# Kernel tuning notes

Hardware: AMD Instinct MI355X
Metric: run time of the kernel (lower is better)

The kernel has to match this reference:

```python
import jax, jax.numpy as jnp
import numpy as np

B, T, C, H = 2, 2048, 1024, 16
D = C // H  # head dim, even
NEG = -1e10  # masked_fill value used by the torch module (not -inf)


def _rope_cache(dim, max_positions):
    # Faithful to source: theta_i = 1/10000**(-2*(i-1)/dim), i = arange(dim//2)
    i = jnp.arange(dim // 2, dtype=jnp.float32)
    theta = 1.0 / (10000.0 ** (-2.0 * (i - 1.0) / dim))
    ang = jnp.arange(max_positions, dtype=jnp.float32)[:, None] * theta[None, :]  # [T, D/2]
    return jnp.cos(ang), jnp.sin(ang)


def _apply_rope(x, cos, sin):
    # x: [B,H,T,D]; consecutive pairs form complex numbers (x[...,2j], x[...,2j+1])
    xp = x.reshape(*x.shape[:-1], D // 2, 2)
    xr, xi = xp[..., 0], xp[..., 1]
    rr = xr * cos - xi * sin
    ri = xr * sin + xi * cos
    return jnp.stack([rr, ri], axis=-1).reshape(x.shape)


def setup_inputs() -> dict:
    key = jax.random.key(0)
    ks = jax.random.split(key, 5)
    s = 1.0 / np.sqrt(C)
    return {
        'x': jax.random.normal(ks[0], (B, T, C), jnp.float32),
        'Wq': jax.random.normal(ks[1], (C, C), jnp.float32) * s,
        'bq': jnp.zeros((C,), jnp.float32),
        'Wk': jax.random.normal(ks[2], (C, C), jnp.float32) * s,
        'bk': jnp.zeros((C,), jnp.float32),
        'Wv': jax.random.normal(ks[3], (C, C), jnp.float32) * s,
        'bv': jnp.zeros((C,), jnp.float32),
        'Wp': jax.random.normal(ks[4], (C, C), jnp.float32) * s,
        'bp': jnp.zeros((C,), jnp.float32),
    }


def reference(x, Wq, bq, Wk, bk, Wv, bv, Wp, bp):
    cos, sin = _rope_cache(D, T)  # [T, D/2]
    def split_heads(h):
        return h.reshape(B, T, H, D).transpose(0, 2, 1, 3)  # [B,H,T,D]
    q = split_heads(x @ Wq.T + bq)
    k = split_heads(x @ Wk.T + bk)
    v = split_heads(x @ Wv.T + bv)
    q = _apply_rope(q, cos, sin)
    k = _apply_rope(k, cos, sin)
    att = jnp.einsum('bhqd,bhkd->bhqk', q, k) * (1.0 / np.sqrt(D))  # [B,H,T,T]
    causal = jnp.tril(jnp.ones((T, T), bool))
    att = jnp.where(causal, att, NEG)
    att = jax.nn.softmax(att, axis=-1)
    y = jnp.einsum('bhqk,bhkd->bhqd', att, v)
    y = y.transpose(0, 2, 1, 3).reshape(B, T, C)
    return y @ Wp.T + bp
```

## Files before the change

kernel.cpp:

```cpp
#include <hip/hip_runtime.h>

#define SEQ 2048
#define CDIM 1024
#define NHEAD 16
#define HDIM 64
#define NSLOT 80

typedef __bf16 bf16x8 __attribute__((ext_vector_type(8)));
typedef __bf16 bf16x4v __attribute__((ext_vector_type(4)));
typedef float f32x4 __attribute__((ext_vector_type(4)));

typedef const __attribute__((address_space(1))) char* gcp_t;
typedef __attribute__((address_space(3))) char* lcp_t;

__device__ __forceinline__ void gload16(const void* g, void* l) {
    __builtin_amdgcn_global_load_lds((gcp_t)g, (lcp_t)l, 16, 0, 0);
}

__device__ __forceinline__ unsigned short f2bf(float f) {
    unsigned int u = __float_as_uint(f);
    u += 0x7fffu + ((u >> 16) & 1u);
    return (unsigned short)(u >> 16);
}

__device__ __forceinline__ float bflo(unsigned int u) { return __uint_as_float(u << 16); }
__device__ __forceinline__ float bfhi(unsigned int u) { return __uint_as_float(u & 0xffff0000u); }

__device__ __forceinline__ int swz16(int r) { return ((r >> 1) & 3) << 4; }


__global__ void cvt_kernel(const float* __restrict__ src, unsigned short* __restrict__ dst, int n4) {
    int i = blockIdx.x * blockDim.x + threadIdx.x;
    if (i < n4) {
        float4 v = ((const float4*)src)[i];
        ushort4 o;
        o.x = f2bf(v.x); o.y = f2bf(v.y); o.z = f2bf(v.z); o.w = f2bf(v.w);
        ((ushort4*)dst)[i] = o;
    }
}

__global__ void cvtw_kernel(const float* __restrict__ Wq, const float* __restrict__ Wk,
                            const float* __restrict__ Wv, const float* __restrict__ Wp,
                            unsigned short* __restrict__ wqkv, unsigned short* __restrict__ wpb) {
    int i = blockIdx.x * blockDim.x + threadIdx.x;
    int which = i >> 18, r = i & 262143;
    const float* s = (which == 0) ? Wq : (which == 1) ? Wk : (which == 2) ? Wv : Wp;
    unsigned short* d = (which < 3) ? (wqkv + (size_t)which * 1048576) : wpb;
    float4 v = ((const float4*)s)[r];
    ushort4 o;
    o.x = f2bf(v.x); o.y = f2bf(v.y); o.z = f2bf(v.z); o.w = f2bf(v.w);
    ((ushort4*)d)[r] = o;
}

__global__ void rope_kernel(float2* __restrict__ cstab) {
    int idx = blockIdx.x * blockDim.x + threadIdx.x;
    int j = idx & 31, t = idx >> 5;
    float e = -2.0f * ((float)j - 1.0f) / 64.0f;
    float denom = (float)pow(10000.0, (double)e);
    float theta = 1.0f / denom;
    float ang = (float)t * theta;
    cstab[idx] = make_float2(cosf(ang), sinf(ang));
}

template <int MODE, int BM, int NXT, int NYT>
__global__ __launch_bounds__(256) void gemm_bt(
    const unsigned short* __restrict__ A, const unsigned short* __restrict__ Bm,
    const float* __restrict__ b0, const float* __restrict__ b1, const float* __restrict__ b2,
    unsigned short* __restrict__ qb, unsigned short* __restrict__ kb,
    unsigned short* __restrict__ vtb, float* __restrict__ outf,
    const float2* __restrict__ cstab)
{
    constexpr int K = 1024;
    constexpr int NIT = K / 32;
    constexpr int NR = (BM == 128) ? 4 : 2;
    constexpr int ABYTES = BM * 64;
    constexpr int BBYTES = 128 * 64;
    __shared__ __align__(16) char As[3][ABYTES];
    __shared__ __align__(16) char Bs[3][BBYTES];
    const int tid = threadIdx.x, lane = tid & 63, wid = tid >> 6;
    constexpr int NWG = NXT * NYT;
    const int bid = blockIdx.x;
    const int swz = (bid & 7) * (NWG >> 3) + (bid >> 3);
    const int mt = swz / NXT;
    const int m0 = mt * BM, n0 = (swz - mt * NXT) * 128;
    const int wr = (BM == 128) ? ((wid >> 1) * 64) : 0;
    const int wc = (BM == 128) ? ((wid & 1) * 64) : (wid * 32);

    f32x4 acc[4][NR] = {};

    const char* Ag = (const char*)(A + (size_t)m0 * K);
    const char* Bg = (const char*)(Bm + (size_t)n0 * K);
    const int r0 = tid >> 2, cb = (tid & 3) * 16;
    const int ldsw = wid << 10;

    auto stage = [&](int k0, int bufi) {
        char* Ad = As[bufi];
        char* Bd = Bs[bufi];
        gload16(Ag + (size_t)r0 * 2048 + k0 * 2 + (cb ^ swz16(r0)), Ad + ldsw);
        if (BM == 128)
            gload16(Ag + (size_t)(r0 + 64) * 2048 + k0 * 2 + (cb ^ swz16(r0 + 64)), Ad + 4096 + ldsw);
        gload16(Bg + (size_t)r0 * 2048 + k0 * 2 + (cb ^ swz16(r0)), Bd + ldsw);
        gload16(Bg + (size_t)(r0 + 64) * 2048 + k0 * 2 + (cb ^ swz16(r0 + 64)), Bd + 4096 + ldsw);
    };

    stage(0, 0);
    stage(32, 1);

    int cur = 0;
    for (int it = 0; it < NIT; ++it) {
        if (it + 1 < NIT) {
            if constexpr (BM == 128) asm volatile("s_waitcnt vmcnt(4)" ::: "memory");
            else                     asm volatile("s_waitcnt vmcnt(3)" ::: "memory");
        } else {
            asm volatile("s_waitcnt vmcnt(0)" ::: "memory");
        }
        __builtin_amdgcn_s_barrier();
        asm volatile("" ::: "memory");
        if (it + 2 < NIT) {
            int nxt2 = cur + 2; if (nxt2 >= 3) nxt2 -= 3;
            stage((it + 2) * 32, nxt2);
        }
        const char* Ac = As[cur];
        const char* Bc = Bs[cur];
        const int fs = (lane >> 4) * 16;
        bf16x8 af[4], bfr[NR];
#pragma unroll
        for (int am = 0; am < 4; ++am) {
            const int r = wr + am * 16 + (lane & 15);
            af[am] = *(const bf16x8*)(Ac + r * 64 + (fs ^ swz16(r)));
        }
#pragma unroll
        for (int an = 0; an < NR; ++an) {
            const int r = wc + an * 16 + (lane & 15);
            bfr[an] = *(const bf16x8*)(Bc + r * 64 + (fs ^ swz16(r)));
        }
#pragma unroll
        for (int am = 0; am < 4; ++am)
#pragma unroll
            for (int an = 0; an < NR; ++an)
                acc[am][an] = __builtin_amdgcn_mfma_f32_16x16x32_bf16(af[am], bfr[an], acc[am][an], 0, 0, 0);
        cur = (cur == 2) ? 0 : cur + 1;
    }

    if (MODE == 0) {
        const float QSCL = 0.18033688011112042f;
#pragma unroll
        for (int an = 0; an < NR; ++an) {
            const int ng = n0 + wc + an * 16 + (lane & 15);
            const int which = ng >> 10, nl = ng & 1023;
            const int h = nl >> 6, d = nl & 63;
            const float* bptr = (which == 0) ? b0 : (which == 1) ? b1 : b2;
            const float bias = bptr[nl];
            if (which < 2) {
                unsigned short* dst = (which == 0) ? qb : kb;
                const float qs = (which == 0) ? QSCL : 1.0f;
                const int j = d >> 1;
#pragma unroll
                for (int am = 0; am < 4; ++am) {
#pragma unroll
                    for (int i = 0; i < 4; ++i) {
                        const int row = m0 + wr + am * 16 + (lane >> 4) * 4 + i;
                        const int bb = row >> 11, t = row & 2047;
                        float v = acc[am][an][i] + bias;
                        float p = __shfl_xor(v, 1);
                        const float2 cs = cstab[t * 32 + j];
                        v = (d & 1) ? fmaf(v, cs.x, p * cs.y) : fmaf(v, cs.x, -p * cs.y);
                        dst[((size_t)((bb * 16 + h) * 2048 + t)) * 64 + d] = f2bf(v * qs);
                    }
                }
            } else {
#pragma unroll
                for (int am = 0; am < 4; ++am) {
                    const int rowb = m0 + wr + am * 16 + (lane >> 4) * 4;
                    const int bb = rowb >> 11, t = rowb & 2047;
                    ushort4 pk;
                    pk.x = f2bf(acc[am][an][0] + bias);
                    pk.y = f2bf(acc[am][an][1] + bias);
                    pk.z = f2bf(acc[am][an][2] + bias);
                    pk.w = f2bf(acc[am][an][3] + bias);
                    *(ushort4*)(vtb + ((size_t)((bb * 16 + h) * 64 + d)) * 2048 + t) = pk;
                }
            }
        }
    } else {
#pragma unroll
        for (int an = 0; an < NR; ++an) {
            const int col = n0 + wc + an * 16 + (lane & 15);
            const float bias = b0[col];
#pragma unroll
            for (int am = 0; am < 4; ++am)
#pragma unroll
                for (int i = 0; i < 4; ++i) {
                    const int row = m0 + wr + am * 16 + (lane >> 4) * 4 + i;
                    outf[(size_t)row * 1024 + col] = acc[am][an][i] + bias;
                }
        }
    }
}

__global__ __launch_bounds__(256) void attn_kernel(
    const unsigned short* __restrict__ qb, const unsigned short* __restrict__ kb,
    const unsigned short* __restrict__ vtb, unsigned short* __restrict__ pb,
    float2* __restrict__ ml)
{
    __shared__ __align__(16) unsigned short Ks[2][64 * 64];
    __shared__ __align__(16) unsigned short Vs[2][64 * 64];
    __shared__ __align__(16) unsigned short Ps[4][16 * 64];
    const int tid = threadIdx.x, lane = tid & 63, wid = tid >> 6;
    const int bh = blockIdx.x;
    const int y = blockIdx.y;
    int qt, ck, nc;
    if (y < 32)      { qt = 31 - (y >> 2); ck = y & 3; nc = 4; }
    else if (y < 56) { int t2 = y - 32; int k3 = t2 / 3; qt = 23 - k3; ck = t2 - k3 * 3; nc = 3; }
    else if (y < 72) { int t2 = y - 56; qt = 15 - (t2 >> 1); ck = t2 & 1; nc = 2; }
    else             { qt = 7 - (y - 72); ck = 0; nc = 1; }
    const int nt = qt + 1;
    const int t0 = ck * nt / nc, t1 = (ck + 1) * nt / nc;
    const int q0 = qt * 64;
    const int qw = q0 + wid * 16;
    const unsigned short* Qg = qb + (size_t)bh * SEQ * HDIM;
    const char* Kg = (const char*)(kb + (size_t)bh * SEQ * HDIM);
    const char* Vg = (const char*)(vtb + (size_t)bh * HDIM * SEQ);

    bf16x8 qf[2];
#pragma unroll
    for (int kf = 0; kf < 2; ++kf)
        qf[kf] = *(const bf16x8*)(Qg + (size_t)(qw + (lane & 15)) * 64 + kf * 32 + (lane >> 4) * 8);

    f32x4 o[4] = {};
    float mrun = -3e38f;
    float lrun = 0.0f;

    const int cr0 = tid >> 3, cc0 = ((tid & 7) * 16) ^ ((cr0 & 7) << 4);
    const int cr1 = cr0 + 32, cc1 = ((tid & 7) * 16) ^ ((cr1 & 7) << 4);
    const int ldsw = wid << 10;

    auto stage = [&](int kt, int bufi) {
        const size_t kv0 = (size_t)kt * 64;
        gload16(Kg + (kv0 + cr0) * 128 + cc0, (char*)Ks[bufi] + ldsw);
        gload16(Kg + (kv0 + cr1) * 128 + cc1, (char*)Ks[bufi] + 4096 + ldsw);
        gload16(Vg + (size_t)cr0 * 4096 + kv0 * 2 + cc0, (char*)Vs[bufi] + ldsw);
        gload16(Vg + (size_t)cr1 * 4096 + kv0 * 2 + cc1, (char*)Vs[bufi] + 4096 + ldsw);
    };

    stage(t0, 0);
    __syncthreads();

    for (int kt = t0; kt < t1; ++kt) {
        const int cur = (kt - t0) & 1;
        if (kt + 1 < t1) stage(kt + 1, cur ^ 1);
        const int kv0 = kt * 64;
        {
            f32x4 s[4] = {};
            __builtin_amdgcn_s_setprio(1);
#pragma unroll
            for (int kf = 0; kf < 2; ++kf) {
                bf16x8 kfr[4];
#pragma unroll
                for (int an = 0; an < 4; ++an) {
                    const int r = an * 16 + (lane & 15);
                    kfr[an] = *(const bf16x8*)((const char*)Ks[cur] + r * 128 + ((kf * 64 + (lane >> 4) * 16) ^ ((r & 7) << 4)));
                }
#pragma unroll
                for (int an = 0; an < 4; ++an)
                    s[an] = __builtin_amdgcn_mfma_f32_16x16x32_bf16(kfr[an], qf[kf], s[an], 0, 0, 0);
            }
            __builtin_amdgcn_s_setprio(0);
            const bool need_mask = (kv0 + 63 > qw);
            const int qg = qw + (lane & 15);
            const int kbase = kv0 + ((lane >> 4) << 2);
            float p[4][4];
            float mx = -3e38f;
#pragma unroll
            for (int an = 0; an < 4; ++an)
#pragma unroll
                for (int i = 0; i < 4; ++i) {
                    float v = s[an][i];
                    if (need_mask && (kbase + an * 16 + i > qg)) v = -3e38f;
                    p[an][i] = v;
                    mx = fmaxf(mx, v);
                }
            mx = fmaxf(mx, __shfl_xor(mx, 16));
            mx = fmaxf(mx, __shfl_xor(mx, 32));
            if (!__all(mx <= mrun + 8.0f)) {
                const float mnew = fmaxf(mrun, mx);
                const float fsc = __builtin_amdgcn_exp2f(mrun - mnew);
                lrun *= fsc;
#pragma unroll
                for (int dn = 0; dn < 4; ++dn) o[dn] *= fsc;
                mrun = mnew;
            }
            float rs = 0.0f;
#pragma unroll
            for (int an = 0; an < 4; ++an)
#pragma unroll
                for (int i = 0; i < 4; ++i) {
                    p[an][i] = __builtin_amdgcn_exp2f(p[an][i] - mrun);
                    rs += p[an][i];
                }
            rs += __shfl_xor(rs, 16);
            rs += __shfl_xor(rs, 32);
            lrun += rs;
            const int ql = lane & 15;
            char* pbs = (char*)Ps[wid] + ql * 128;
            const int xr = (ql & 7) << 4;
            const int gb = (lane >> 4) << 3;
#pragma unroll
            for (int an = 0; an < 4; ++an) {
                bf16x4v pk;
                pk[0] = (__bf16)p[an][0]; pk[1] = (__bf16)p[an][1];
                pk[2] = (__bf16)p[an][2]; pk[3] = (__bf16)p[an][3];
                *(bf16x4v*)(pbs + ((an * 32 + gb) ^ xr)) = pk;
            }
            __builtin_amdgcn_s_setprio(1);
#pragma unroll
            for (int kf = 0; kf < 2; ++kf) {
                bf16x8 vf[4], pf;
#pragma unroll
                for (int dn = 0; dn < 4; ++dn) {
                    const int r = dn * 16 + (lane & 15);
                    vf[dn] = *(const bf16x8*)((const char*)Vs[cur] + r * 128 + ((kf * 64 + (lane >> 4) * 16) ^ ((r & 7) << 4)));
                }
                {
                    const int qlr = lane & 15;
                    pf = *(const bf16x8*)((const char*)Ps[wid] + qlr * 128 + ((kf * 64 + (lane >> 4) * 16) ^ ((qlr & 7) << 4)));
                }
#pragma unroll
                for (int dn = 0; dn < 4; ++dn)
                    o[dn] = __builtin_amdgcn_mfma_f32_16x16x32_bf16(vf[dn], pf, o[dn], 0, 0, 0);
            }
            __builtin_amdgcn_s_setprio(0);
        }
        __syncthreads();
    }

    {
        const size_t sbase = (size_t)bh * NSLOT + y;
        const int qloc = wid * 16 + (lane & 15);
        unsigned short* prow = pb + (sbase * 64 + qloc) * 64;
#pragma unroll
        for (int dn = 0; dn < 4; ++dn) {
            const int d = dn * 16 + ((lane >> 4) << 2);
            bf16x4v pk;
            pk[0] = (__bf16)o[dn][0];
            pk[1] = (__bf16)o[dn][1];
            pk[2] = (__bf16)o[dn][2];
            pk[3] = (__bf16)o[dn][3];
            *(bf16x4v*)(prow + d) = pk;
        }
        if ((lane >> 4) == 0) ml[sbase * 64 + qloc] = make_float2(mrun, lrun);
    }
}

__global__ __launch_bounds__(256) void combine_kernel(
    const unsigned short* __restrict__ pb, const float2* __restrict__ ml,
    unsigned short* __restrict__ yb)
{
    const int qt = blockIdx.x, bh = blockIdx.y;
    const int b = bh >> 4, h = bh & 15;
    int base, nc;
    if (qt >= 24)      { base = (31 - qt) * 4;      nc = 4; }
    else if (qt >= 16) { base = 32 + (23 - qt) * 3; nc = 3; }
    else if (qt >= 8)  { base = 56 + (15 - qt) * 2; nc = 2; }
    else               { base = 72 + (7 - qt);      nc = 1; }
    const int t = threadIdx.x;
    const int q = t >> 2;
    const int d0 = (t & 3) * 16;
    const size_t sbase = (size_t)bh * NSLOT + base;

    float m[4], l[4];
    float M = -3e38f;
#pragma unroll
    for (int c = 0; c < 4; ++c)
        if (c < nc) {
            float2 v = ml[(sbase + c) * 64 + q];
            m[c] = v.x; l[c] = v.y;
            M = fmaxf(M, v.x);
        }
    float L = 0.0f;
    float w[4];
#pragma unroll
    for (int c = 0; c < 4; ++c)
        if (c < nc) {
            w[c] = __builtin_amdgcn_exp2f(m[c] - M);
            L += l[c] * w[c];
        }
    const float invL = 1.0f / L;

    float acc[16] = {};
#pragma unroll
    for (int c = 0; c < 4; ++c)
        if (c < nc) {
            const float wc = w[c] * invL;
            const uint4* src = (const uint4*)(pb + ((sbase + c) * 64 + q) * 64 + d0);
            uint4 A = src[0], B = src[1];
            const unsigned int ua[8] = {A.x, A.y, A.z, A.w, B.x, B.y, B.z, B.w};
#pragma unroll
            for (int k = 0; k < 8; ++k) {
                acc[2 * k]     = fmaf(wc, bflo(ua[k]), acc[2 * k]);
                acc[2 * k + 1] = fmaf(wc, bfhi(ua[k]), acc[2 * k + 1]);
            }
        }

    unsigned int outw[8];
#pragma unroll
    for (int k = 0; k < 8; ++k)
        outw[k] = (unsigned int)f2bf(acc[2 * k]) | ((unsigned int)f2bf(acc[2 * k + 1]) << 16);
    uint4* dst = (uint4*)(yb + (size_t)(b * SEQ + qt * 64 + q) * CDIM + h * 64 + d0);
    dst[0] = make_uint4(outw[0], outw[1], outw[2], outw[3]);
    dst[1] = make_uint4(outw[4], outw[5], outw[6], outw[7]);
}


extern "C" void kernel_launch(void* const* d_in, const int* in_sizes, int n_in,
                              void* d_out, int out_size, void* d_ws, size_t ws_size,
                              hipStream_t stream) {
    (void)in_sizes; (void)n_in; (void)out_size; (void)ws_size;
    const float* x  = (const float*)d_in[0];
    const float* Wq = (const float*)d_in[1];
    const float* bq = (const float*)d_in[2];
    const float* Wk = (const float*)d_in[3];
    const float* bk = (const float*)d_in[4];
    const float* Wv = (const float*)d_in[5];
    const float* bv = (const float*)d_in[6];
    const float* Wp = (const float*)d_in[7];
    const float* bp = (const float*)d_in[8];
    float* out = (float*)d_out;

    char* ws = (char*)d_ws;
    size_t off = 0;
    auto take = [&](size_t bytes) -> char* {
        char* p = ws + off;
        off = (off + bytes + 255) & ~(size_t)255;
        return p;
    };
    float2* cstab = (float2*)take((size_t)SEQ * 32 * 8);
    unsigned short* xb   = (unsigned short*)take((size_t)4096 * 1024 * 2);
    unsigned short* wqkv = (unsigned short*)take((size_t)3 * 1024 * 1024 * 2);
    unsigned short* wpb  = (unsigned short*)take((size_t)1024 * 1024 * 2);
    unsigned short* qbuf = (unsigned short*)take((size_t)32 * SEQ * HDIM * 2);
    unsigned short* kbuf = (unsigned short*)take((size_t)32 * SEQ * HDIM * 2);
    unsigned short* vtb  = (unsigned short*)take((size_t)32 * HDIM * SEQ * 2);
    unsigned short* yb   = (unsigned short*)take((size_t)4096 * 1024 * 2);
    unsigned short* pbuf = (unsigned short*)take((size_t)32 * NSLOT * 64 * 64 * 2);
    float2* mlb          = (float2*)take((size_t)32 * NSLOT * 64 * 8);

    rope_kernel<<<256, 256, 0, stream>>>(cstab);
    cvt_kernel<<<4096, 256, 0, stream>>>(x, xb, 1048576);
    cvtw_kernel<<<4096, 256, 0, stream>>>(Wq, Wk, Wv, Wp, wqkv, wpb);

    gemm_bt<0, 128, 24, 32><<<768, 256, 0, stream>>>(xb, wqkv, bq, bk, bv, qbuf, kbuf, vtb, nullptr, cstab);
    dim3 g1(32, NSLOT);
    attn_kernel<<<g1, 256, 0, stream>>>(qbuf, kbuf, vtb, pbuf, mlb);
    dim3 gc(32, 32);
    combine_kernel<<<gc, 256, 0, stream>>>(pbuf, mlb, yb);
    gemm_bt<1, 64, 8, 64><<<512, 256, 0, stream>>>(yb, wpb, bp, nullptr, nullptr, nullptr, nullptr, nullptr, out, cstab);
}
```

Measured before the change: 146.8 us.

## Use 128-row query tiles in attention and simplify GEMM pipeline to double buffering

The attention kernel now gives each wave 32 query rows instead of 16, so every K/V tile loaded into shared memory serves twice as many queries and the split-KV slot count halves. Key tiles lying entirely above a wave's diagonal are skipped. The GEMM drops its 3-stage pipeline with manual vmcnt waits and its block-index swizzle, going back to a 2-stage double buffer with __syncthreads and a plain 2D grid. The GEMM change gives up load/compute overlap and L2 locality, and the larger attention tiles raise register pressure and lower the block count.

```diff
diff --git a/kernel.cpp b/kernel.cpp
--- a/kernel.cpp
+++ b/kernel.cpp
@@ -4,7 +4,7 @@
 #define CDIM 1024
 #define NHEAD 16
 #define HDIM 64
-#define NSLOT 80
+#define NSLOT 40
 
 typedef __bf16 bf16x8 __attribute__((ext_vector_type(8)));
 typedef __bf16 bf16x4v __attribute__((ext_vector_type(4)));
@@ -62,7 +62,7 @@
     cstab[idx] = make_float2(cosf(ang), sinf(ang));
 }
 
-template <int MODE, int BM, int NXT, int NYT>
+template <int MODE, int BM>
 __global__ __launch_bounds__(256) void gemm_bt(
     const unsigned short* __restrict__ A, const unsigned short* __restrict__ Bm,
     const float* __restrict__ b0, const float* __restrict__ b1, const float* __restrict__ b2,
@@ -73,16 +73,10 @@
     constexpr int K = 1024;
     constexpr int NIT = K / 32;
     constexpr int NR = (BM == 128) ? 4 : 2;
-    constexpr int ABYTES = BM * 64;
-    constexpr int BBYTES = 128 * 64;
-    __shared__ __align__(16) char As[3][ABYTES];
-    __shared__ __align__(16) char Bs[3][BBYTES];
+    __shared__ __align__(16) char As[2][BM * 64];
+    __shared__ __align__(16) char Bs[2][128 * 64];
     const int tid = threadIdx.x, lane = tid & 63, wid = tid >> 6;
-    constexpr int NWG = NXT * NYT;
-    const int bid = blockIdx.x;
-    const int swz = (bid & 7) * (NWG >> 3) + (bid >> 3);
-    const int mt = swz / NXT;
-    const int m0 = mt * BM, n0 = (swz - mt * NXT) * 128;
+    const int m0 = blockIdx.y * BM, n0 = blockIdx.x * 128;
     const int wr = (BM == 128) ? ((wid >> 1) * 64) : 0;
     const int wc = (BM == 128) ? ((wid & 1) * 64) : (wid * 32);
 
@@ -97,29 +91,18 @@
         char* Ad = As[bufi];
         char* Bd = Bs[bufi];
         gload16(Ag + (size_t)r0 * 2048 + k0 * 2 + (cb ^ swz16(r0)), Ad + ldsw);
-        if (BM == 128)
+        if constexpr (BM == 128)
             gload16(Ag + (size_t)(r0 + 64) * 2048 + k0 * 2 + (cb ^ swz16(r0 + 64)), Ad + 4096 + ldsw);
         gload16(Bg + (size_t)r0 * 2048 + k0 * 2 + (cb ^ swz16(r0)), Bd + ldsw);
         gload16(Bg + (size_t)(r0 + 64) * 2048 + k0 * 2 + (cb ^ swz16(r0 + 64)), Bd + 4096 + ldsw);
     };
 
     stage(0, 0);
-    stage(32, 1);
-
-    int cur = 0;
+    __syncthreads();
+
     for (int it = 0; it < NIT; ++it) {
-        if (it + 1 < NIT) {
-            if constexpr (BM == 128) asm volatile("s_waitcnt vmcnt(4)" ::: "memory");
-            else                     asm volatile("s_waitcnt vmcnt(3)" ::: "memory");
-        } else {
-            asm volatile("s_waitcnt vmcnt(0)" ::: "memory");
-        }
-        __builtin_amdgcn_s_barrier();
-        asm volatile("" ::: "memory");
-        if (it + 2 < NIT) {
-            int nxt2 = cur + 2; if (nxt2 >= 3) nxt2 -= 3;
-            stage((it + 2) * 32, nxt2);
-        }
+        const int cur = it & 1;
+        if (it + 1 < NIT) stage((it + 1) * 32, cur ^ 1);
         const char* Ac = As[cur];
         const char* Bc = Bs[cur];
         const int fs = (lane >> 4) * 16;
@@ -139,7 +122,7 @@
 #pragma unroll
             for (int an = 0; an < NR; ++an)
                 acc[am][an] = __builtin_amdgcn_mfma_f32_16x16x32_bf16(af[am], bfr[an], acc[am][an], 0, 0, 0);
-        cur = (cur == 2) ? 0 : cur + 1;
+        __syncthreads();
     }
 
     if (MODE == 0) {
@@ -205,31 +188,33 @@
 {
     __shared__ __align__(16) unsigned short Ks[2][64 * 64];
     __shared__ __align__(16) unsigned short Vs[2][64 * 64];
-    __shared__ __align__(16) unsigned short Ps[4][16 * 64];
+    __shared__ __align__(16) unsigned short Ps[4][32 * 64];
     const int tid = threadIdx.x, lane = tid & 63, wid = tid >> 6;
     const int bh = blockIdx.x;
     const int y = blockIdx.y;
     int qt, ck, nc;
-    if (y < 32)      { qt = 31 - (y >> 2); ck = y & 3; nc = 4; }
-    else if (y < 56) { int t2 = y - 32; int k3 = t2 / 3; qt = 23 - k3; ck = t2 - k3 * 3; nc = 3; }
-    else if (y < 72) { int t2 = y - 56; qt = 15 - (t2 >> 1); ck = t2 & 1; nc = 2; }
-    else             { qt = 7 - (y - 72); ck = 0; nc = 1; }
-    const int nt = qt + 1;
+    if (y < 16)      { qt = 15 - (y >> 2); ck = y & 3; nc = 4; }
+    else if (y < 28) { int t2 = y - 16; int k3 = t2 / 3; qt = 11 - k3; ck = t2 - k3 * 3; nc = 3; }
+    else if (y < 36) { int t2 = y - 28; qt = 7 - (t2 >> 1); ck = t2 & 1; nc = 2; }
+    else             { qt = 3 - (y - 36); ck = 0; nc = 1; }
+    const int nt = 2 * qt + 2;
     const int t0 = ck * nt / nc, t1 = (ck + 1) * nt / nc;
-    const int q0 = qt * 64;
-    const int qw = q0 + wid * 16;
+    const int q0 = qt * 128;
+    const int qw = q0 + wid * 32;
     const unsigned short* Qg = qb + (size_t)bh * SEQ * HDIM;
     const char* Kg = (const char*)(kb + (size_t)bh * SEQ * HDIM);
     const char* Vg = (const char*)(vtb + (size_t)bh * HDIM * SEQ);
 
-    bf16x8 qf[2];
-#pragma unroll
-    for (int kf = 0; kf < 2; ++kf)
-        qf[kf] = *(const bf16x8*)(Qg + (size_t)(qw + (lane & 15)) * 64 + kf * 32 + (lane >> 4) * 8);
-
-    f32x4 o[4] = {};
-    float mrun = -3e38f;
-    float lrun = 0.0f;
+    bf16x8 qf[2][2];
+#pragma unroll
+    for (int am = 0; am < 2; ++am)
+#pragma unroll
+        for (int kf = 0; kf < 2; ++kf)
+            qf[am][kf] = *(const bf16x8*)(Qg + (size_t)(qw + am * 16 + (lane & 15)) * 64 + kf * 32 + (lane >> 4) * 8);
+
+    f32x4 o[4][2] = {};
+    float mrun[2] = {-3e38f, -3e38f};
+    float lrun[2] = {0.0f, 0.0f};
 
     const int cr0 = tid >> 3, cc0 = ((tid & 7) * 16) ^ ((cr0 & 7) << 4);
     const int cr1 = cr0 + 32, cc1 = ((tid & 7) * 16) ^ ((cr1 & 7) << 4);
@@ -250,8 +235,8 @@
         const int cur = (kt - t0) & 1;
         if (kt + 1 < t1) stage(kt + 1, cur ^ 1);
         const int kv0 = kt * 64;
-        {
-            f32x4 s[4] = {};
+        if (kv0 <= qw + 31) {
+            f32x4 s[4][2] = {};
             __builtin_amdgcn_s_setprio(1);
 #pragma unroll
             for (int kf = 0; kf < 2; ++kf) {
@@ -263,71 +248,79 @@
                 }
 #pragma unroll
                 for (int an = 0; an < 4; ++an)
-                    s[an] = __builtin_amdgcn_mfma_f32_16x16x32_bf16(kfr[an], qf[kf], s[an], 0, 0, 0);
+#pragma unroll
+                    for (int am = 0; am < 2; ++am)
+                        s[an][am] = __builtin_amdgcn_mfma_f32_16x16x32_bf16(kfr[an], qf[am][kf], s[an][am], 0, 0, 0);
             }
             __builtin_amdgcn_s_setprio(0);
             const bool need_mask = (kv0 + 63 > qw);
-            const int qg = qw + (lane & 15);
-            const int kbase = kv0 + ((lane >> 4) << 2);
-            float p[4][4];
-            float mx = -3e38f;
-#pragma unroll
-            for (int an = 0; an < 4; ++an)
-#pragma unroll
-                for (int i = 0; i < 4; ++i) {
-                    float v = s[an][i];
-                    if (need_mask && (kbase + an * 16 + i > qg)) v = -3e38f;
-                    p[an][i] = v;
-                    mx = fmaxf(mx, v);
-                }
-            mx = fmaxf(mx, __shfl_xor(mx, 16));
-            mx = fmaxf(mx, __shfl_xor(mx, 32));
-            if (!__all(mx <= mrun + 8.0f)) {
-                const float mnew = fmaxf(mrun, mx);
-                const float fsc = __builtin_amdgcn_exp2f(mrun - mnew);
-                lrun *= fsc;
-#pragma unroll
-                for (int dn = 0; dn < 4; ++dn) o[dn] *= fsc;
-                mrun = mnew;
-            }
-            float rs = 0.0f;
-#pragma unroll
-            for (int an = 0; an < 4; ++an)
-#pragma unroll
-                for (int i = 0; i < 4; ++i) {
-                    p[an][i] = __builtin_amdgcn_exp2f(p[an][i] - mrun);
-                    rs += p[an][i];
-                }
-            rs += __shfl_xor(rs, 16);
-            rs += __shfl_xor(rs, 32);
-            lrun += rs;
-            const int ql = lane & 15;
-            char* pbs = (char*)Ps[wid] + ql * 128;
-            const int xr = (ql & 7) << 4;
-            const int gb = (lane >> 4) << 3;
-#pragma unroll
-            for (int an = 0; an < 4; ++an) {
-                bf16x4v pk;
-                pk[0] = (__bf16)p[an][0]; pk[1] = (__bf16)p[an][1];
-                pk[2] = (__bf16)p[an][2]; pk[3] = (__bf16)p[an][3];
-                *(bf16x4v*)(pbs + ((an * 32 + gb) ^ xr)) = pk;
+#pragma unroll
+            for (int am = 0; am < 2; ++am) {
+                const int qg = qw + am * 16 + (lane & 15);
+                const int kbase = kv0 + ((lane >> 4) << 2);
+                float p[4][4];
+                float mx = -3e38f;
+#pragma unroll
+                for (int an = 0; an < 4; ++an)
+#pragma unroll
+                    for (int i = 0; i < 4; ++i) {
+                        float v = s[an][am][i];
+                        if (need_mask && (kbase + an * 16 + i > qg)) v = -3e38f;
+                        p[an][i] = v;
+                        mx = fmaxf(mx, v);
+                    }
+                mx = fmaxf(mx, __shfl_xor(mx, 16));
+                mx = fmaxf(mx, __shfl_xor(mx, 32));
+                if (!__all(mx <= mrun[am] + 8.0f)) {
+                    const float mnew = fmaxf(mrun[am], mx);
+                    const float fsc = __builtin_amdgcn_exp2f(mrun[am] - mnew);
+                    lrun[am] *= fsc;
+#pragma unroll
+                    for (int dn = 0; dn < 4; ++dn) o[dn][am] *= fsc;
+                    mrun[am] = mnew;
+                }
+                float rs = 0.0f;
+#pragma unroll
+                for (int an = 0; an < 4; ++an)
+#pragma unroll
+                    for (int i = 0; i < 4; ++i) {
+                        p[an][i] = __builtin_amdgcn_exp2f(p[an][i] - mrun[am]);
+                        rs += p[an][i];
+                    }
+                rs += __shfl_xor(rs, 16);
+                rs += __shfl_xor(rs, 32);
+                lrun[am] += rs;
+                const int ql = am * 16 + (lane & 15);
+                char* pbs = (char*)Ps[wid] + ql * 128;
+                const int xr = (ql & 7) << 4;
+                const int gb = (lane >> 4) << 3;
+#pragma unroll
+                for (int an = 0; an < 4; ++an) {
+                    bf16x4v pk;
+                    pk[0] = (__bf16)p[an][0]; pk[1] = (__bf16)p[an][1];
+                    pk[2] = (__bf16)p[an][2]; pk[3] = (__bf16)p[an][3];
+                    *(bf16x4v*)(pbs + ((an * 32 + gb) ^ xr)) = pk;
+                }
             }
             __builtin_amdgcn_s_setprio(1);
 #pragma unroll
             for (int kf = 0; kf < 2; ++kf) {
-                bf16x8 vf[4], pf;
+                bf16x8 vf[4], pf[2];
 #pragma unroll
                 for (int dn = 0; dn < 4; ++dn) {
                     const int r = dn * 16 + (lane & 15);
                     vf[dn] = *(const bf16x8*)((const char*)Vs[cur] + r * 128 + ((kf * 64 + (lane >> 4) * 16) ^ ((r & 7) << 4)));
                 }
-                {
-                    const int qlr = lane & 15;
-                    pf = *(const bf16x8*)((const char*)Ps[wid] + qlr * 128 + ((kf * 64 + (lane >> 4) * 16) ^ ((qlr & 7) << 4)));
+#pragma unroll
+                for (int am = 0; am < 2; ++am) {
+                    const int ql = am * 16 + (lane & 15);
+                    pf[am] = *(const bf16x8*)((const char*)Ps[wid] + ql * 128 + ((kf * 64 + (lane >> 4) * 16) ^ ((ql & 7) << 4)));
                 }
 #pragma unroll
                 for (int dn = 0; dn < 4; ++dn)
-                    o[dn] = __builtin_amdgcn_mfma_f32_16x16x32_bf16(vf[dn], pf, o[dn], 0, 0, 0);
+#pragma unroll
+                    for (int am = 0; am < 2; ++am)
+                        o[dn][am] = __builtin_amdgcn_mfma_f32_16x16x32_bf16(vf[dn], pf[am], o[dn][am], 0, 0, 0);
             }
             __builtin_amdgcn_s_setprio(0);
         }
@@ -336,19 +329,22 @@
 
     {
         const size_t sbase = (size_t)bh * NSLOT + y;
-        const int qloc = wid * 16 + (lane & 15);
-        unsigned short* prow = pb + (sbase * 64 + qloc) * 64;
-#pragma unroll
-        for (int dn = 0; dn < 4; ++dn) {
-            const int d = dn * 16 + ((lane >> 4) << 2);
-            bf16x4v pk;
-            pk[0] = (__bf16)o[dn][0];
-            pk[1] = (__bf16)o[dn][1];
-            pk[2] = (__bf16)o[dn][2];
-            pk[3] = (__bf16)o[dn][3];
-            *(bf16x4v*)(prow + d) = pk;
-        }
-        if ((lane >> 4) == 0) ml[sbase * 64 + qloc] = make_float2(mrun, lrun);
+#pragma unroll
+        for (int am = 0; am < 2; ++am) {
+            const int qloc = wid * 32 + am * 16 + (lane & 15);
+            unsigned short* prow = pb + (sbase * 128 + qloc) * 64;
+#pragma unroll
+            for (int dn = 0; dn < 4; ++dn) {
+                const int d = dn * 16 + ((lane >> 4) << 2);
+                bf16x4v pk;
+                pk[0] = (__bf16)o[dn][am][0];
+                pk[1] = (__bf16)o[dn][am][1];
+                pk[2] = (__bf16)o[dn][am][2];
+                pk[3] = (__bf16)o[dn][am][3];
+                *(bf16x4v*)(prow + d) = pk;
+            }
+            if ((lane >> 4) == 0) ml[sbase * 128 + qloc] = make_float2(mrun[am], lrun[am]);
+        }
     }
 }
 
@@ -356,15 +352,16 @@
     const unsigned short* __restrict__ pb, const float2* __restrict__ ml,
     unsigned short* __restrict__ yb)
 {
-    const int qt = blockIdx.x, bh = blockIdx.y;
+    const int bx = blockIdx.x, bh = blockIdx.y;
+    const int qt = bx >> 1, qh = (bx & 1) * 64;
     const int b = bh >> 4, h = bh & 15;
     int base, nc;
-    if (qt >= 24)      { base = (31 - qt) * 4;      nc = 4; }
-    else if (qt >= 16) { base = 32 + (23 - qt) * 3; nc = 3; }
-    else if (qt >= 8)  { base = 56 + (15 - qt) * 2; nc = 2; }
-    else               { base = 72 + (7 - qt);      nc = 1; }
+    if (qt >= 12)      { base = (15 - qt) * 4;      nc = 4; }
+    else if (qt >= 8)  { base = 16 + (11 - qt) * 3; nc = 3; }
+    else if (qt >= 4)  { base = 28 + (7 - qt) * 2;  nc = 2; }
+    else               { base = 36 + (3 - qt);      nc = 1; }
     const int t = threadIdx.x;
-    const int q = t >> 2;
+    const int q = qh + (t >> 2);
     const int d0 = (t & 3) * 16;
     const size_t sbase = (size_t)bh * NSLOT + base;
 
@@ -373,7 +370,7 @@
 #pragma unroll
     for (int c = 0; c < 4; ++c)
         if (c < nc) {
-            float2 v = ml[(sbase + c) * 64 + q];
+            float2 v = ml[(sbase + c) * 128 + q];
             m[c] = v.x; l[c] = v.y;
             M = fmaxf(M, v.x);
         }
@@ -392,7 +389,7 @@
     for (int c = 0; c < 4; ++c)
         if (c < nc) {
             const float wc = w[c] * invL;
-            const uint4* src = (const uint4*)(pb + ((sbase + c) * 64 + q) * 64 + d0);
+            const uint4* src = (const uint4*)(pb + ((sbase + c) * 128 + q) * 64 + d0);
             uint4 A = src[0], B = src[1];
             const unsigned int ua[8] = {A.x, A.y, A.z, A.w, B.x, B.y, B.z, B.w};
 #pragma unroll
@@ -406,7 +403,7 @@
 #pragma unroll
     for (int k = 0; k < 8; ++k)
         outw[k] = (unsigned int)f2bf(acc[2 * k]) | ((unsigned int)f2bf(acc[2 * k + 1]) << 16);
-    uint4* dst = (uint4*)(yb + (size_t)(b * SEQ + qt * 64 + q) * CDIM + h * 64 + d0);
+    uint4* dst = (uint4*)(yb + (size_t)(b * SEQ + qt * 128 + q) * CDIM + h * 64 + d0);
     dst[0] = make_uint4(outw[0], outw[1], outw[2], outw[3]);
     dst[1] = make_uint4(outw[4], outw[5], outw[6], outw[7]);
 }
@@ -442,17 +439,19 @@
     unsigned short* kbuf = (unsigned short*)take((size_t)32 * SEQ * HDIM * 2);
     unsigned short* vtb  = (unsigned short*)take((size_t)32 * HDIM * SEQ * 2);
     unsigned short* yb   = (unsigned short*)take((size_t)4096 * 1024 * 2);
-    unsigned short* pbuf = (unsigned short*)take((size_t)32 * NSLOT * 64 * 64 * 2);
-    float2* mlb          = (float2*)take((size_t)32 * NSLOT * 64 * 8);
+    unsigned short* pbuf = (unsigned short*)take((size_t)32 * NSLOT * 128 * 64 * 2);
+    float2* mlb          = (float2*)take((size_t)32 * NSLOT * 128 * 8);
 
     rope_kernel<<<256, 256, 0, stream>>>(cstab);
     cvt_kernel<<<4096, 256, 0, stream>>>(x, xb, 1048576);
     cvtw_kernel<<<4096, 256, 0, stream>>>(Wq, Wk, Wv, Wp, wqkv, wpb);
 
-    gemm_bt<0, 128, 24, 32><<<768, 256, 0, stream>>>(xb, wqkv, bq, bk, bv, qbuf, kbuf, vtb, nullptr, cstab);
+    dim3 g0(24, 32);
+    gemm_bt<0, 128><<<g0, 256, 0, stream>>>(xb, wqkv, bq, bk, bv, qbuf, kbuf, vtb, nullptr, cstab);
     dim3 g1(32, NSLOT);
     attn_kernel<<<g1, 256, 0, stream>>>(qbuf, kbuf, vtb, pbuf, mlb);
     dim3 gc(32, 32);
     combine_kernel<<<gc, 256, 0, stream>>>(pbuf, mlb, yb);
-    gemm_bt<1, 64, 8, 64><<<512, 256, 0, stream>>>(yb, wpb, bp, nullptr, nullptr, nullptr, nullptr, nullptr, out, cstab);
-}
+    dim3 g2(8, 64);
+    gemm_bt<1, 64><<<g2, 256, 0, stream>>>(yb, wpb, bp, nullptr, nullptr, nullptr, nullptr, nullptr, out, cstab);
+}
```

New measurement: 142.3 us. 3.1% less time.
